# Kernel optimization log

Hardware: AMD Instinct MI355X
Metric: run time of the kernel (lower is better)

Reference implementation:

```python
import jax, jax.numpy as jnp
import numpy as np

DIN = 1024
DOUT = 1024

def setup_inputs() -> dict:
    key = jax.random.key(0)
    kx, kq, kk, kv = jax.random.split(key, 4)
    x = jax.random.normal(kx, (4, 2048, DIN), dtype=jnp.float32)
    s = 1.0 / np.sqrt(DIN)
    Wq = jax.random.uniform(kq, (DIN, DOUT), dtype=jnp.float32, minval=-s, maxval=s)
    Wk = jax.random.uniform(kk, (DIN, DOUT), dtype=jnp.float32, minval=-s, maxval=s)
    Wv = jax.random.uniform(kv, (DIN, DOUT), dtype=jnp.float32, minval=-s, maxval=s)
    return {"x": x, "Wq": Wq, "Wk": Wk, "Wv": Wv}

def reference(x, Wq, Wk, Wv):
    # q,k,v: [B, T, D]
    q = jnp.einsum('btd,de->bte', x, Wq)
    k = jnp.einsum('btd,de->bte', x, Wk)
    v = jnp.einsum('btd,de->bte', x, Wv)
    # scores: [B, T_q, T_k]; NOTE: no 1/sqrt(d) scaling in original
    scores = jnp.einsum('bqd,bkd->bqk', q, k)
    # Original applies softmax over dim=1 (the QUERY axis), faithfully kept
    weights = jax.nn.softmax(scores, axis=1)
    return jnp.einsum('bqk,bkd->bqd', weights, v)
```

## Files before the change

### kernel.cpp

```cpp
#include <hip/hip_runtime.h>

#define B_   4
#define T_   2048
#define D_   1024
#define MTOK 8192

typedef __attribute__((ext_vector_type(8))) _Float16 half8;
typedef __attribute__((ext_vector_type(4))) float    f32x4;

#define GLD(G, L) __builtin_amdgcn_global_load_lds(                       \
    (const __attribute__((address_space(1))) void*)(G),                   \
    (__attribute__((address_space(3))) void*)(L), 16, 0, 0)

#define BAR()   __builtin_amdgcn_s_barrier()
#define BARM()  asm volatile("s_barrier" ::: "memory")
#define LGKM0() do { asm volatile("s_waitcnt lgkmcnt(0)" ::: "memory");   \
                     __builtin_amdgcn_sched_barrier(0); } while (0)
#define VMW(n)  asm volatile("s_waitcnt vmcnt(" #n ")" ::: "memory")

__device__ __forceinline__ unsigned short f2h(float f) {
  return __builtin_bit_cast(unsigned short, (_Float16)f);
}
__device__ __forceinline__ float h2f(unsigned short u) {
  return (float)__builtin_bit_cast(_Float16, u);
}

__global__ __launch_bounds__(256) void tofp16_kernel(
    const float4* __restrict__ in, ushort4* __restrict__ out, int n4,
    float4* __restrict__ cs, int c4) {
  int i = blockIdx.x * 256 + threadIdx.x;
  if (i < c4) cs[i] = (float4){0.f, 0.f, 0.f, 0.f};
  if (i >= n4) return;
  float4 v = in[i];
  ushort4 h;
  h.x = f2h(v.x); h.y = f2h(v.y); h.z = f2h(v.z); h.w = f2h(v.w);
  out[i] = h;
}

__global__ __launch_bounds__(256) void wcat_t_kernel(
    const float* __restrict__ Wq, const float* __restrict__ Wk,
    const float* __restrict__ Wv, unsigned short* __restrict__ Wt) {
  __shared__ float tile[32][33];
  int z = blockIdx.z;
  const float* W = (z == 0) ? Wq : ((z == 1) ? Wk : Wv);
  int c0 = blockIdx.x * 32, r0 = blockIdx.y * 32;
  int tx = threadIdx.x & 31, ty = threadIdx.x >> 5;
  #pragma unroll
  for (int i = 0; i < 4; ++i)
    tile[ty + i * 8][tx] = W[(size_t)(r0 + ty + i * 8) * D_ + c0 + tx];
  __syncthreads();
  #pragma unroll
  for (int i = 0; i < 4; ++i) {
    float v = tile[tx][ty + i * 8];
    size_t row = (size_t)z * D_ + c0 + ty + i * 8;
    Wt[row * D_ + r0 + tx] = f2h(v);
  }
}

__global__ __launch_bounds__(256) void vtrans_kernel(
    const unsigned short* __restrict__ QKV, unsigned short* __restrict__ Vt) {
  __shared__ unsigned short tile[64][68];
  int b = blockIdx.z;
  int t0 = blockIdx.x * 64, d0 = blockIdx.y * 64;
  int l16 = threadIdx.x & 15, rr = threadIdx.x >> 4;
  const unsigned short* src =
      QKV + ((size_t)b * 2048 + t0 + rr) * 3072 + 2048 + d0 + l16 * 4;
  #pragma unroll
  for (int i = 0; i < 4; ++i) {
    ushort4 v = *(const ushort4*)(src + (size_t)i * 16 * 3072);
    *(ushort4*)&tile[rr + i * 16][l16 * 4] = v;
  }
  __syncthreads();
  unsigned short* dst = Vt + ((size_t)b * D_ + d0) * 2048 + t0;
  #pragma unroll
  for (int j = 0; j < 4; ++j) {
    int dd = rr + j * 16;
    int tt = l16 * 4;
    ushort4 v;
    v.x = tile[tt + 0][dd]; v.y = tile[tt + 1][dd];
    v.z = tile[tt + 2][dd]; v.w = tile[tt + 3][dd];
    *(ushort4*)(dst + (size_t)dd * 2048 + tt) = v;
  }
}

template <int EPI>
__global__ __launch_bounds__(512, 4) void gemm8p(
    const unsigned short* __restrict__ A, const unsigned short* __restrict__ B,
    void* __restrict__ C0, float* __restrict__ CS,
    int K, int lda, int ldb, int ldc,
    long aBatch, long bBatch, long cBatch) {
  constexpr int ABY  = 128 * 64;
  constexpr int BUFB = ABY + 16384;
  __shared__ __align__(16) char lds[2 * BUFB];

  const int z = blockIdx.z;
  A += (size_t)z * aBatch;
  B += (size_t)z * bBatch;

  const int nwg = gridDim.x * gridDim.y;
  int s = blockIdx.y * gridDim.x + blockIdx.x;
  s = (s & 7) * (nwg >> 3) + (s >> 3);
  const int bx = s % gridDim.x, by = s / gridDim.x;
  const int brow = by * 128, bcol = bx * 256;

  const int tid = threadIdx.x;
  const int wid = tid >> 6, lane = tid & 63;
  const int wr = wid >> 2, wc = wid & 3;
  const int l15 = lane & 15, g4 = lane >> 4;

  const int scol = ((lane & 3) ^ ((lane >> 3) & 3)) * 8;
  const int srow = lane >> 2;
  int aoff, adst, boffs[2], bdst[2];
  {
    int r0 = wid * 16;
    aoff = (brow + r0 + srow) * lda + scol;
    adst = r0 * 64;
    #pragma unroll
    for (int rg = 0; rg < 2; ++rg) {
      int rb = (wid >> 1) * 64 + rg * 32 + (wid & 1) * 16;
      boffs[rg] = (bcol + rb + srow) * ldb + scol;
      bdst[rg]  = ABY + rb * 64;
    }
  }

  const int rslot = (g4 ^ ((l15 >> 1) & 3)) * 16;
  int aRd[2], bRd[2];
  #pragma unroll
  for (int mh = 0; mh < 2; ++mh) {
    aRd[mh] = (wr * 64 + mh * 32 + l15) * 64 + rslot;
    bRd[mh] = ABY + (wc * 64 + mh * 32 + l15) * 64 + rslot;
  }

#define STAGE_A(bb, tt) \
    GLD(A + (size_t)(aoff + (tt) * 32), lds + (bb) * BUFB + adst)
#define STAGE_B(nh, bb, tt) \
    GLD(B + (size_t)(boffs[nh] + (tt) * 32), lds + (bb) * BUFB + bdst[nh])
#define LOAD_A(mh) do { _Pragma("unroll")                                     \
    for (int mf = 0; mf < 2; ++mf)                                            \
      ar[mf] = *(const half8*)(buf + aRd[mh] + mf * 1024); } while (0)
#define LOAD_B(dst, nh) do { _Pragma("unroll")                                \
    for (int nf = 0; nf < 2; ++nf)                                            \
      dst[nf] = *(const half8*)(buf + bRd[nh] + nf * 1024); } while (0)
#define MFMA_Q(mh, nh, br) do { _Pragma("unroll")                             \
    for (int mf = 0; mf < 2; ++mf) { _Pragma("unroll")                        \
      for (int nf = 0; nf < 2; ++nf) {                                        \
        f32x4& ac = acc[(mh) * 2 + mf][(nh) * 2 + nf];                        \
        ac = __builtin_amdgcn_mfma_f32_16x16x32_f16(ar[mf], br[nf], ac, 0, 0, 0); \
      } } } while (0)

  STAGE_A(0, 0); STAGE_B(0, 0, 0); STAGE_B(1, 0, 0);
  STAGE_A(1, 1); STAGE_B(0, 1, 1); STAGE_B(1, 1, 1);
  VMW(3);
  BAR();

  f32x4 acc[4][4] = {};
  half8 ar[2], b0r[2], b1r[2];
  const int nIter = K / 64;

  for (int it = 0; it < nIter; ++it) {
    const bool st = (it + 1 < nIter);
    #pragma unroll
    for (int h = 0; h < 2; ++h) {
      const char* buf = lds + h * BUFB;
      const int tt = 2 * it + 2 + h;
      LOAD_A(0); LOAD_B(b0r, 0);
      BAR(); LGKM0();
      __builtin_amdgcn_s_setprio(1); MFMA_Q(0, 0, b0r);
      __builtin_amdgcn_s_setprio(0); BAR();
      LOAD_B(b1r, 1);
      if (st) STAGE_B(0, h, tt);
      BAR(); LGKM0();
      __builtin_amdgcn_s_setprio(1); MFMA_Q(0, 1, b1r);
      __builtin_amdgcn_s_setprio(0); BAR();
      LOAD_A(1);
      if (st) STAGE_B(1, h, tt);
      BAR(); LGKM0();
      __builtin_amdgcn_s_setprio(1); MFMA_Q(1, 1, b1r);
      __builtin_amdgcn_s_setprio(0); BAR();
      if (st) STAGE_A(h, tt);
      BAR();
      __builtin_amdgcn_s_setprio(1); MFMA_Q(1, 0, b0r);
      __builtin_amdgcn_s_setprio(0);
      if (st) { VMW(3); } else { VMW(0); }
      BAR();
    }
  }

  if constexpr (EPI == 1) {
    unsigned short* C = (unsigned short*)C0 + (size_t)z * cBatch;
    #pragma unroll
    for (int m = 0; m < 4; ++m) {
      int rowoff = (m >> 1) * 32 + (m & 1) * 16;
      #pragma unroll
      for (int n = 0; n < 4; ++n) {
        int coloff = (n >> 1) * 32 + (n & 1) * 16;
        #pragma unroll
        for (int r = 0; r < 4; ++r) {
          int row = brow + wr * 64 + rowoff + g4 * 4 + r;
          int col = bcol + wc * 64 + coloff + l15;
          C[(size_t)row * ldc + col] = f2h(acc[m][n][r]);
        }
      }
    }
  } else {
    unsigned short* C = (unsigned short*)C0 + (size_t)z * cBatch;
    float csum[4] = {0.f, 0.f, 0.f, 0.f};
    #pragma unroll
    for (int m = 0; m < 4; ++m) {
      int rowoff = (m >> 1) * 32 + (m & 1) * 16;
      #pragma unroll
      for (int n = 0; n < 4; ++n) {
        int coloff = (n >> 1) * 32 + (n & 1) * 16;
        #pragma unroll
        for (int r = 0; r < 4; ++r) {
          int row = brow + wr * 64 + rowoff + g4 * 4 + r;
          int col = bcol + wc * 64 + coloff + l15;
          unsigned short hh = f2h(acc[m][n][r]);
          C[(size_t)row * ldc + col] = hh;
          csum[n] += __expf(h2f(hh) - 64.0f);
        }
      }
    }
    #pragma unroll
    for (int n = 0; n < 4; ++n) {
      csum[n] += __shfl_xor(csum[n], 16);
      csum[n] += __shfl_xor(csum[n], 32);
    }
    if (g4 == 0) {
      #pragma unroll
      for (int n = 0; n < 4; ++n) {
        int col = bcol + wc * 64 + (n >> 1) * 32 + (n & 1) * 16 + l15;
        unsafeAtomicAdd(CS + (size_t)z * T_ + col, csum[n]);
      }
    }
  }
#undef STAGE_A
#undef STAGE_B
#undef LOAD_A
#undef LOAD_B
#undef MFMA_Q
}

__global__ __launch_bounds__(256, 2) void gemmPV(
    const unsigned short* __restrict__ Sc, const float* __restrict__ U,
    const unsigned short* __restrict__ Bv, float* __restrict__ out) {
  constexpr int ABY  = 64 * 64;
  constexpr int BUFB = ABY + 16384;
  __shared__ __align__(16) char lds[3 * BUFB];

  const int b = blockIdx.z;
  Sc += (size_t)b * T_ * T_;
  U  += (size_t)b * T_;
  Bv += (size_t)b * D_ * T_;
  float* Co = out + (size_t)b * T_ * D_;

  const int nwg = gridDim.x * gridDim.y;
  int s = blockIdx.y * gridDim.x + blockIdx.x;
  s = (s & 7) * (nwg >> 3) + (s >> 3);
  const int bx = s % gridDim.x, by = s / gridDim.x;
  const int brow = by * 64, bcol = bx * 256;

  const int tid = threadIdx.x;
  const int wid = tid >> 6, lane = tid & 63;
  const int l15 = lane & 15, g4 = lane >> 4;

  const int arow = tid >> 2;
  const unsigned short* aSrc = Sc + (size_t)(brow + arow) * T_ + (tid & 3) * 8;
  const int awB  = arow * 64 + ((tid & 3) ^ ((tid >> 3) & 3)) * 16;
  const int ucol = (tid & 3) * 8;

  const int scol = ((lane & 3) ^ ((lane >> 3) & 3)) * 8;
  const int srow = lane >> 2;
  int boffs[4], bdst[4];
  #pragma unroll
  for (int g = 0; g < 4; ++g) {
    int rb = g * 64 + wid * 16;
    boffs[g] = (bcol + rb + srow) * T_ + scol;
    bdst[g]  = ABY + rb * 64;
  }

  const int rslot = (g4 ^ ((l15 >> 1) & 3)) * 16;
  int aRd[4], bRd[4];
  #pragma unroll
  for (int mf = 0; mf < 4; ++mf)
    aRd[mf] = (mf * 16 + l15) * 64 + rslot;
  #pragma unroll
  for (int nf = 0; nf < 4; ++nf)
    bRd[nf] = ABY + (wid * 64 + nf * 16 + l15) * 64 + rslot;

  uint4 rawA;
  float4 uva, uvb;

#define PV_BSTAGE(base, tt) do { _Pragma("unroll")                            \
    for (int g = 0; g < 4; ++g)                                               \
      GLD(Bv + (size_t)(boffs[g] + (tt) * 32), (base) + bdst[g]); } while (0)
#define PV_AISSUE(tt) do {                                                    \
    rawA = *(const uint4*)(aSrc + (size_t)(tt) * 32);                         \
    uva  = *(const float4*)(U + (tt) * 32 + ucol);                            \
    uvb  = *(const float4*)(U + (tt) * 32 + ucol + 4); } while (0)
#define PV_AWRITE(base) do {                                                  \
    const unsigned short* hp = (const unsigned short*)&rawA;                  \
    float uu[8] = {uva.x, uva.y, uva.z, uva.w, uvb.x, uvb.y, uvb.z, uvb.w};   \
    unsigned int w_[4];                                                       \
    _Pragma("unroll") for (int j = 0; j < 4; ++j) {                           \
      float w0 = __expf(h2f(hp[2 * j])     - 64.f) * uu[2 * j];               \
      float w1 = __expf(h2f(hp[2 * j + 1]) - 64.f) * uu[2 * j + 1];           \
      w_[j] = (unsigned int)f2h(w0) | ((unsigned int)f2h(w1) << 16); }        \
    *(uint4*)((base) + awB) = *(uint4*)w_; } while (0)

  char* bufA = lds;
  char* bufB = lds + BUFB;
  char* bufC = lds + 2 * BUFB;

  PV_AISSUE(0);
  PV_BSTAGE(bufA, 0);
  uint4  rawA1 = *(const uint4*)(aSrc + 32);
  float4 uva1  = *(const float4*)(U + 32 + ucol);
  float4 uvb1  = *(const float4*)(U + 32 + ucol + 4);
  PV_BSTAGE(bufB, 1);
  VMW(11);
  PV_AWRITE(bufA);
  VMW(4);
  rawA = rawA1; uva = uva1; uvb = uvb1;
  PV_AWRITE(bufB);
  asm volatile("s_waitcnt lgkmcnt(0)" ::: "memory");

  f32x4 acc[4][4] = {};
  half8 ar[4], br[4];
  const int NT = T_ / 32;

  for (int t = 0; t < NT; ++t) {
    BARM();
    const bool st = (t + 2 < NT);
    if (st) {
      PV_AISSUE(t + 2);
      PV_BSTAGE(bufC, t + 2);
    }
    #pragma unroll
    for (int mf = 0; mf < 4; ++mf)
      ar[mf] = *(const half8*)(bufA + aRd[mf]);
    #pragma unroll
    for (int nf = 0; nf < 4; ++nf)
      br[nf] = *(const half8*)(bufA + bRd[nf]);
    __builtin_amdgcn_s_setprio(1);
    #pragma unroll
    for (int mf = 0; mf < 4; ++mf)
      #pragma unroll
      for (int nf = 0; nf < 4; ++nf)
        acc[mf][nf] = __builtin_amdgcn_mfma_f32_16x16x32_f16(ar[mf], br[nf], acc[mf][nf], 0, 0, 0);
    __builtin_amdgcn_s_setprio(0);
    if (st) {
      VMW(4);
      PV_AWRITE(bufC);
      asm volatile("s_waitcnt lgkmcnt(0)" ::: "memory");
    } else if (t + 2 == NT) {
      VMW(0);
    }
    char* tmp = bufA; bufA = bufB; bufB = bufC; bufC = tmp;
  }

  #pragma unroll
  for (int mf = 0; mf < 4; ++mf)
    #pragma unroll
    for (int nf = 0; nf < 4; ++nf)
      #pragma unroll
      for (int r = 0; r < 4; ++r) {
        int row = brow + mf * 16 + g4 * 4 + r;
        int col = bcol + wid * 64 + nf * 16 + l15;
        Co[(size_t)row * D_ + col] = acc[mf][nf][r];
      }
#undef PV_BSTAGE
#undef PV_AISSUE
#undef PV_AWRITE
}

__global__ __launch_bounds__(256) void sm_stats(const float* __restrict__ cs,
                                                float* __restrict__ stats) {
  int i = blockIdx.x * 256 + threadIdx.x;
  stats[i] = 1.0f / cs[i];
}

extern "C" void kernel_launch(void* const* d_in, const int* in_sizes, int n_in,
                              void* d_out, int out_size, void* d_ws, size_t ws_size,
                              hipStream_t stream) {
  const float* x  = (const float*)d_in[0];
  const float* Wq = (const float*)d_in[1];
  const float* Wk = (const float*)d_in[2];
  const float* Wv = (const float*)d_in[3];
  float* out = (float*)d_out;

  char* ws = (char*)d_ws;
  const size_t MB = 1024ull * 1024ull;
  unsigned short* scoresh = (unsigned short*)(ws);
  unsigned short* QKVh = (unsigned short*)(ws + 32 * MB);
  unsigned short* Vt   = (unsigned short*)(ws + 80 * MB);
  unsigned short* xh   = (unsigned short*)(ws + 96 * MB);
  unsigned short* Wt   = (unsigned short*)(ws + 112 * MB);
  float* colsum = (float*)(ws + 118 * MB);
  float* stats  = (float*)(ws + 118 * MB + 64 * 1024);

  tofp16_kernel<<<MTOK * D_ / 4 / 256, 256, 0, stream>>>(
      (const float4*)x, (ushort4*)xh, MTOK * D_ / 4,
      (float4*)colsum, B_ * T_ / 4);

  wcat_t_kernel<<<dim3(32, 32, 3), 256, 0, stream>>>(Wq, Wk, Wv, Wt);

  gemm8p<1><<<dim3(3072 / 256, MTOK / 128, 1), 512, 0, stream>>>(
      xh, Wt, QKVh, nullptr, D_, D_, D_, 3072, 0, 0, 0);

  vtrans_kernel<<<dim3(T_ / 64, D_ / 64, B_), 256, 0, stream>>>(QKVh, Vt);

  gemm8p<2><<<dim3(T_ / 256, T_ / 128, B_), 512, 0, stream>>>(
      QKVh, QKVh + 1024, scoresh, colsum, D_, 3072, 3072, T_,
      (long)T_ * 3072, (long)T_ * 3072, (long)T_ * T_);

  sm_stats<<<B_ * T_ / 256, 256, 0, stream>>>(colsum, stats);

  gemmPV<<<dim3(D_ / 256, T_ / 64, B_), 256, 0, stream>>>(
      scoresh, stats, Vt, out);
}
```

Measured before the change: 198.3 us.

## Add dedicated 128x128 scores GEMM and deepen PV A-operand prefetch

Replaces the 256x128, 512-thread gemm8p instantiation for the QK^T scores with a new 256-thread 128x128-tile kernel, gemmS. It uses a three-buffer global_load_lds pipeline, targets three blocks per CU, and keeps the fused column-sum/atomic epilogue. gemmPV now prefetches the softmax-weight operand one tile further ahead into registers, using a two-tile unrolled loop with alternating register sets, so global latency is hidden behind the MFMAs. This trades more registers and a smaller tile with less reuse for better occupancy and deeper latency hiding.

```diff
diff --git a/kernel.cpp b/kernel.cpp
--- a/kernel.cpp
+++ b/kernel.cpp
@@ -186,51 +186,18 @@
     }
   }
 
-  if constexpr (EPI == 1) {
-    unsigned short* C = (unsigned short*)C0 + (size_t)z * cBatch;
-    #pragma unroll
-    for (int m = 0; m < 4; ++m) {
-      int rowoff = (m >> 1) * 32 + (m & 1) * 16;
+  unsigned short* C = (unsigned short*)C0 + (size_t)z * cBatch;
+  #pragma unroll
+  for (int m = 0; m < 4; ++m) {
+    int rowoff = (m >> 1) * 32 + (m & 1) * 16;
+    #pragma unroll
+    for (int n = 0; n < 4; ++n) {
+      int coloff = (n >> 1) * 32 + (n & 1) * 16;
       #pragma unroll
-      for (int n = 0; n < 4; ++n) {
-        int coloff = (n >> 1) * 32 + (n & 1) * 16;
-        #pragma unroll
-        for (int r = 0; r < 4; ++r) {
-          int row = brow + wr * 64 + rowoff + g4 * 4 + r;
-          int col = bcol + wc * 64 + coloff + l15;
-          C[(size_t)row * ldc + col] = f2h(acc[m][n][r]);
-        }
-      }
-    }
-  } else {
-    unsigned short* C = (unsigned short*)C0 + (size_t)z * cBatch;
-    float csum[4] = {0.f, 0.f, 0.f, 0.f};
-    #pragma unroll
-    for (int m = 0; m < 4; ++m) {
-      int rowoff = (m >> 1) * 32 + (m & 1) * 16;
-      #pragma unroll
-      for (int n = 0; n < 4; ++n) {
-        int coloff = (n >> 1) * 32 + (n & 1) * 16;
-        #pragma unroll
-        for (int r = 0; r < 4; ++r) {
-          int row = brow + wr * 64 + rowoff + g4 * 4 + r;
-          int col = bcol + wc * 64 + coloff + l15;
-          unsigned short hh = f2h(acc[m][n][r]);
-          C[(size_t)row * ldc + col] = hh;
-          csum[n] += __expf(h2f(hh) - 64.0f);
-        }
-      }
-    }
-    #pragma unroll
-    for (int n = 0; n < 4; ++n) {
-      csum[n] += __shfl_xor(csum[n], 16);
-      csum[n] += __shfl_xor(csum[n], 32);
-    }
-    if (g4 == 0) {
-      #pragma unroll
-      for (int n = 0; n < 4; ++n) {
-        int col = bcol + wc * 64 + (n >> 1) * 32 + (n & 1) * 16 + l15;
-        unsafeAtomicAdd(CS + (size_t)z * T_ + col, csum[n]);
+      for (int r = 0; r < 4; ++r) {
+        int row = brow + wr * 64 + rowoff + g4 * 4 + r;
+        int col = bcol + wc * 64 + coloff + l15;
+        C[(size_t)row * ldc + col] = f2h(acc[m][n][r]);
       }
     }
   }
@@ -239,6 +206,119 @@
 #undef LOAD_A
 #undef LOAD_B
 #undef MFMA_Q
+}
+
+__global__ __launch_bounds__(256, 3) void gemmS(
+    const unsigned short* __restrict__ A, const unsigned short* __restrict__ B,
+    unsigned short* __restrict__ C0, float* __restrict__ CS,
+    int K, int lda, int ldb, int ldc,
+    long aBatch, long bBatch, long cBatch) {
+  constexpr int ABY  = 128 * 64;
+  constexpr int BUFB = ABY + 8192;
+  __shared__ __align__(16) char lds[3 * BUFB];
+
+  const int z = blockIdx.z;
+  A += (size_t)z * aBatch;
+  B += (size_t)z * bBatch;
+
+  const int nwg = gridDim.x * gridDim.y;
+  int s = blockIdx.y * gridDim.x + blockIdx.x;
+  s = (s & 7) * (nwg >> 3) + (s >> 3);
+  const int bx = s % gridDim.x, by = s / gridDim.x;
+  const int brow = by * 128, bcol = bx * 128;
+
+  const int tid = threadIdx.x;
+  const int wid = tid >> 6, lane = tid & 63;
+  const int wr = wid >> 1, wc = wid & 1;
+  const int l15 = lane & 15, g4 = lane >> 4;
+
+  const int scol = ((lane & 3) ^ ((lane >> 3) & 3)) * 8;
+  const int srow = lane >> 2;
+  int aoffs[2], adst[2], boffs[2], bdst[2];
+  #pragma unroll
+  for (int g = 0; g < 2; ++g) {
+    int r0 = wid * 32 + g * 16;
+    aoffs[g] = (brow + r0 + srow) * lda + scol;
+    adst[g]  = r0 * 64;
+    boffs[g] = (bcol + r0 + srow) * ldb + scol;
+    bdst[g]  = ABY + r0 * 64;
+  }
+
+  const int rslot = (g4 ^ ((l15 >> 1) & 3)) * 16;
+  int aRd[4], bRd[4];
+  #pragma unroll
+  for (int mf = 0; mf < 4; ++mf)
+    aRd[mf] = (wr * 64 + mf * 16 + l15) * 64 + rslot;
+  #pragma unroll
+  for (int nf = 0; nf < 4; ++nf)
+    bRd[nf] = ABY + (wc * 64 + nf * 16 + l15) * 64 + rslot;
+
+#define S_STAGE(base, tt) do { _Pragma("unroll")                              \
+    for (int g = 0; g < 2; ++g) {                                             \
+      GLD(A + (size_t)(aoffs[g] + (tt) * 32), (base) + adst[g]);              \
+      GLD(B + (size_t)(boffs[g] + (tt) * 32), (base) + bdst[g]); } } while (0)
+
+  char* bufA = lds;
+  char* bufB = lds + BUFB;
+  char* bufC = lds + 2 * BUFB;
+
+  S_STAGE(bufA, 0);
+  S_STAGE(bufB, 1);
+  VMW(4);
+
+  f32x4 acc[4][4] = {};
+  half8 ar[4], br[4];
+  const int NT = K / 32;
+
+  for (int t = 0; t < NT; ++t) {
+    BARM();
+    const bool st = (t + 2 < NT);
+    if (st) S_STAGE(bufC, t + 2);
+    #pragma unroll
+    for (int mf = 0; mf < 4; ++mf)
+      ar[mf] = *(const half8*)(bufA + aRd[mf]);
+    #pragma unroll
+    for (int nf = 0; nf < 4; ++nf)
+      br[nf] = *(const half8*)(bufA + bRd[nf]);
+    __builtin_amdgcn_s_setprio(1);
+    #pragma unroll
+    for (int mf = 0; mf < 4; ++mf)
+      #pragma unroll
+      for (int nf = 0; nf < 4; ++nf)
+        acc[mf][nf] = __builtin_amdgcn_mfma_f32_16x16x32_f16(ar[mf], br[nf], acc[mf][nf], 0, 0, 0);
+    __builtin_amdgcn_s_setprio(0);
+    if (st)                VMW(4);
+    else if (t + 2 == NT)  VMW(0);
+    char* tmp = bufA; bufA = bufB; bufB = bufC; bufC = tmp;
+  }
+
+  unsigned short* C = C0 + (size_t)z * cBatch;
+  float csum[4] = {0.f, 0.f, 0.f, 0.f};
+  #pragma unroll
+  for (int mf = 0; mf < 4; ++mf)
+    #pragma unroll
+    for (int nf = 0; nf < 4; ++nf)
+      #pragma unroll
+      for (int r = 0; r < 4; ++r) {
+        int row = brow + wr * 64 + mf * 16 + g4 * 4 + r;
+        int col = bcol + wc * 64 + nf * 16 + l15;
+        unsigned short hh = f2h(acc[mf][nf][r]);
+        C[(size_t)row * ldc + col] = hh;
+        csum[nf] += __expf(h2f(hh) - 64.0f);
+      }
+  #pragma unroll
+  for (int nf = 0; nf < 4; ++nf) {
+    csum[nf] += __shfl_xor(csum[nf], 16);
+    csum[nf] += __shfl_xor(csum[nf], 32);
+  }
+  if (g4 == 0) {
+    #pragma unroll
+    for (int nf = 0; nf < 4; ++nf) {
+      int col = bcol + wc * 64 + nf * 16 + l15;
+      unsafeAtomicAdd(CS + (size_t)z * T_ + col, csum[nf]);
+    }
+  }
+#undef S_STAGE
 }
 
 __global__ __launch_bounds__(256, 2) void gemmPV(
@@ -288,75 +368,73 @@
   for (int nf = 0; nf < 4; ++nf)
     bRd[nf] = ABY + (wid * 64 + nf * 16 + l15) * 64 + rslot;
 
-  uint4 rawA;
-  float4 uva, uvb;
-
 #define PV_BSTAGE(base, tt) do { _Pragma("unroll")                            \
     for (int g = 0; g < 4; ++g)                                               \
       GLD(Bv + (size_t)(boffs[g] + (tt) * 32), (base) + bdst[g]); } while (0)
-#define PV_AISSUE(tt) do {                                                    \
-    rawA = *(const uint4*)(aSrc + (size_t)(tt) * 32);                         \
-    uva  = *(const float4*)(U + (tt) * 32 + ucol);                            \
-    uvb  = *(const float4*)(U + (tt) * 32 + ucol + 4); } while (0)
-#define PV_AWRITE(base) do {                                                  \
-    const unsigned short* hp = (const unsigned short*)&rawA;                  \
-    float uu[8] = {uva.x, uva.y, uva.z, uva.w, uvb.x, uvb.y, uvb.z, uvb.w};   \
+#define PV_ALOAD(rA, uA, uB, tt) do {                                         \
+    rA = *(const uint4*)(aSrc + (size_t)(tt) * 32);                           \
+    uA = *(const float4*)(U + (tt) * 32 + ucol);                              \
+    uB = *(const float4*)(U + (tt) * 32 + ucol + 4); } while (0)
+#define PV_AWRITE(base, rA, uA, uB) do {                                      \
+    const unsigned short* hp = (const unsigned short*)&rA;                    \
+    float uu[8] = {uA.x, uA.y, uA.z, uA.w, uB.x, uB.y, uB.z, uB.w};           \
     unsigned int w_[4];                                                       \
     _Pragma("unroll") for (int j = 0; j < 4; ++j) {                           \
       float w0 = __expf(h2f(hp[2 * j])     - 64.f) * uu[2 * j];               \
       float w1 = __expf(h2f(hp[2 * j + 1]) - 64.f) * uu[2 * j + 1];           \
       w_[j] = (unsigned int)f2h(w0) | ((unsigned int)f2h(w1) << 16); }        \
     *(uint4*)((base) + awB) = *(uint4*)w_; } while (0)
+#define PV_COMPUTE() do {                                                     \
+    _Pragma("unroll") for (int mf = 0; mf < 4; ++mf)                          \
+      ar[mf] = *(const half8*)(bufA + aRd[mf]);                               \
+    _Pragma("unroll") for (int nf = 0; nf < 4; ++nf)                          \
+      br[nf] = *(const half8*)(bufA + bRd[nf]);                               \
+    __builtin_amdgcn_s_setprio(1);                                            \
+    _Pragma("unroll") for (int mf = 0; mf < 4; ++mf)                          \
+      _Pragma("unroll") for (int nf = 0; nf < 4; ++nf)                        \
+        acc[mf][nf] = __builtin_amdgcn_mfma_f32_16x16x32_f16(                 \
+            ar[mf], br[nf], acc[mf][nf], 0, 0, 0);                            \
+    __builtin_amdgcn_s_setprio(0); } while (0)
+#define PV_TILE(t, rC, uCa, uCb, rN, uNa, uNb) do {                           \
+    BARM();                                                                   \
+    if ((t) + 2 < NT) PV_BSTAGE(bufC, (t) + 2);                               \
+    if ((t) + 3 < NT) PV_ALOAD(rN, uNa, uNb, (t) + 3);                        \
+    PV_COMPUTE();                                                             \
+    if ((t) + 3 < NT)      VMW(7);                                            \
+    else if ((t) + 2 < NT) VMW(4);                                            \
+    else if ((t) + 2 == NT) VMW(0);                                           \
+    if ((t) + 2 < NT) {                                                       \
+      PV_AWRITE(bufC, rC, uCa, uCb);                                          \
+      asm volatile("s_waitcnt lgkmcnt(0)" ::: "memory");                      \
+    }                                                                         \
+    { char* tmp = bufA; bufA = bufB; bufB = bufC; bufC = tmp; } } while (0)
 
   char* bufA = lds;
   char* bufB = lds + BUFB;
   char* bufC = lds + 2 * BUFB;
 
-  PV_AISSUE(0);
+  uint4 rA_E, rA_O; float4 uAa_E, uAb_E, uAa_O, uAb_O;
+
+  uint4 rA0; float4 uA0a, uA0b;
+  PV_ALOAD(rA0, uA0a, uA0b, 0);
   PV_BSTAGE(bufA, 0);
-  uint4  rawA1 = *(const uint4*)(aSrc + 32);
-  float4 uva1  = *(const float4*)(U + 32 + ucol);
-  float4 uvb1  = *(const float4*)(U + 32 + ucol + 4);
+  uint4 rA1; float4 uA1a, uA1b;
+  PV_ALOAD(rA1, uA1a, uA1b, 1);
   PV_BSTAGE(bufB, 1);
-  VMW(11);
-  PV_AWRITE(bufA);
-  VMW(4);
-  rawA = rawA1; uva = uva1; uvb = uvb1;
-  PV_AWRITE(bufB);
+  PV_ALOAD(rA_O, uAa_O, uAb_O, 2);
+  VMW(14);
+  PV_AWRITE(bufA, rA0, uA0a, uA0b);
+  VMW(7);
+  PV_AWRITE(bufB, rA1, uA1a, uA1b);
   asm volatile("s_waitcnt lgkmcnt(0)" ::: "memory");
 
   f32x4 acc[4][4] = {};
   half8 ar[4], br[4];
   const int NT = T_ / 32;
 
-  for (int t = 0; t < NT; ++t) {
-    BARM();
-    const bool st = (t + 2 < NT);
-    if (st) {
-      PV_AISSUE(t + 2);
-      PV_BSTAGE(bufC, t + 2);
-    }
-    #pragma unroll
-    for (int mf = 0; mf < 4; ++mf)
-      ar[mf] = *(const half8*)(bufA + aRd[mf]);
-    #pragma unroll
-    for (int nf = 0; nf < 4; ++nf)
-      br[nf] = *(const half8*)(bufA + bRd[nf]);
-    __builtin_amdgcn_s_setprio(1);
-    #pragma unroll
-    for (int mf = 0; mf < 4; ++mf)
-      #pragma unroll
-      for (int nf = 0; nf < 4; ++nf)
-        acc[mf][nf] = __builtin_amdgcn_mfma_f32_16x16x32_f16(ar[mf], br[nf], acc[mf][nf], 0, 0, 0);
-    __builtin_amdgcn_s_setprio(0);
-    if (st) {
-      VMW(4);
-      PV_AWRITE(bufC);
-      asm volatile("s_waitcnt lgkmcnt(0)" ::: "memory");
-    } else if (t + 2 == NT) {
-      VMW(0);
-    }
-    char* tmp = bufA; bufA = bufB; bufB = bufC; bufC = tmp;
+  for (int t = 0; t < NT; t += 2) {
+    PV_TILE(t,     rA_O, uAa_O, uAb_O, rA_E, uAa_E, uAb_E);
+    PV_TILE(t + 1, rA_E, uAa_E, uAb_E, rA_O, uAa_O, uAb_O);
   }
 
   #pragma unroll
@@ -370,8 +448,10 @@
         Co[(size_t)row * D_ + col] = acc[mf][nf][r];
       }
 #undef PV_BSTAGE
-#undef PV_AISSUE
+#undef PV_ALOAD
 #undef PV_AWRITE
+#undef PV_COMPUTE
+#undef PV_TILE
 }
 
 __global__ __launch_bounds__(256) void sm_stats(const float* __restrict__ cs,
@@ -410,7 +490,7 @@
 
   vtrans_kernel<<<dim3(T_ / 64, D_ / 64, B_), 256, 0, stream>>>(QKVh, Vt);
 
-  gemm8p<2><<<dim3(T_ / 256, T_ / 128, B_), 512, 0, stream>>>(
+  gemmS<<<dim3(T_ / 128, T_ / 128, B_), 256, 0, stream>>>(
       QKVh, QKVh + 1024, scoresh, colsum, D_, 3072, 3072, T_,
       (long)T_ * 3072, (long)T_ * 3072, (long)T_ * T_);
 
```

Measured after the change: 207.7 us. 1.05x slower.

## Transpose PV GEMM tiling so scores load straight to registers with LDS-staged output

Applied to the files above, without the earlier changes.

The PV kernel now tiles over 256 query rows by 64 output features per block. The score tiles are loaded directly into registers as the MFMA B operand, and the exp-and-scale step runs in registers, so scores are no longer staged through LDS. Only Vt is staged in LDS through a three-buffer ring, and results are transposed through LDS for coalesced float4 stores. This aims to cut LDS traffic and footprint on the larger operand and to vectorise the output writes, at the cost of uncoalesced 16-byte register loads of scores and extra barriers in the epilogue.

```diff
diff --git a/kernel.cpp b/kernel.cpp
--- a/kernel.cpp
+++ b/kernel.cpp
@@ -241,137 +241,129 @@
 #undef MFMA_Q
 }
 
-__global__ __launch_bounds__(256, 2) void gemmPV(
+__global__ __launch_bounds__(256, 2) void gemmPVt(
     const unsigned short* __restrict__ Sc, const float* __restrict__ U,
-    const unsigned short* __restrict__ Bv, float* __restrict__ out) {
-  constexpr int ABY  = 64 * 64;
-  constexpr int BUFB = ABY + 16384;
-  __shared__ __align__(16) char lds[3 * BUFB];
+    const unsigned short* __restrict__ Vt, float* __restrict__ out) {
+  constexpr int BUFB = 4096;
+  __shared__ __align__(16) char lds[34816];
 
   const int b = blockIdx.z;
   Sc += (size_t)b * T_ * T_;
   U  += (size_t)b * T_;
-  Bv += (size_t)b * D_ * T_;
+  Vt += (size_t)b * D_ * T_;
   float* Co = out + (size_t)b * T_ * D_;
 
   const int nwg = gridDim.x * gridDim.y;
   int s = blockIdx.y * gridDim.x + blockIdx.x;
   s = (s & 7) * (nwg >> 3) + (s >> 3);
   const int bx = s % gridDim.x, by = s / gridDim.x;
-  const int brow = by * 64, bcol = bx * 256;
+  const int q0 = bx * 256, d0 = by * 64;
 
   const int tid = threadIdx.x;
   const int wid = tid >> 6, lane = tid & 63;
   const int l15 = lane & 15, g4 = lane >> 4;
 
-  const int arow = tid >> 2;
-  const unsigned short* aSrc = Sc + (size_t)(brow + arow) * T_ + (tid & 3) * 8;
-  const int awB  = arow * 64 + ((tid & 3) ^ ((tid >> 3) & 3)) * 16;
-  const int ucol = (tid & 3) * 8;
-
   const int scol = ((lane & 3) ^ ((lane >> 3) & 3)) * 8;
-  const int srow = lane >> 2;
-  int boffs[4], bdst[4];
-  #pragma unroll
-  for (int g = 0; g < 4; ++g) {
-    int rb = g * 64 + wid * 16;
-    boffs[g] = (bcol + rb + srow) * T_ + scol;
-    bdst[g]  = ABY + rb * 64;
-  }
+  const int aoff = (d0 + wid * 16 + (lane >> 2)) * T_ + scol;
+  const int adst = wid * 1024;
 
   const int rslot = (g4 ^ ((l15 >> 1) & 3)) * 16;
-  int aRd[4], bRd[4];
+  int aRd[4];
   #pragma unroll
   for (int mf = 0; mf < 4; ++mf)
     aRd[mf] = (mf * 16 + l15) * 64 + rslot;
+
+  const unsigned short* bSrc[4];
   #pragma unroll
   for (int nf = 0; nf < 4; ++nf)
-    bRd[nf] = ABY + (wid * 64 + nf * 16 + l15) * 64 + rslot;
-
-  uint4 rawA;
-  float4 uva, uvb;
-
-#define PV_BSTAGE(base, tt) do { _Pragma("unroll")                            \
-    for (int g = 0; g < 4; ++g)                                               \
-      GLD(Bv + (size_t)(boffs[g] + (tt) * 32), (base) + bdst[g]); } while (0)
-#define PV_AISSUE(tt) do {                                                    \
-    rawA = *(const uint4*)(aSrc + (size_t)(tt) * 32);                         \
-    uva  = *(const float4*)(U + (tt) * 32 + ucol);                            \
-    uvb  = *(const float4*)(U + (tt) * 32 + ucol + 4); } while (0)
-#define PV_AWRITE(base) do {                                                  \
-    const unsigned short* hp = (const unsigned short*)&rawA;                  \
-    float uu[8] = {uva.x, uva.y, uva.z, uva.w, uvb.x, uvb.y, uvb.z, uvb.w};   \
-    unsigned int w_[4];                                                       \
-    _Pragma("unroll") for (int j = 0; j < 4; ++j) {                           \
-      float w0 = __expf(h2f(hp[2 * j])     - 64.f) * uu[2 * j];               \
-      float w1 = __expf(h2f(hp[2 * j + 1]) - 64.f) * uu[2 * j + 1];           \
-      w_[j] = (unsigned int)f2h(w0) | ((unsigned int)f2h(w1) << 16); }        \
-    *(uint4*)((base) + awB) = *(uint4*)w_; } while (0)
+    bSrc[nf] = Sc + (size_t)(q0 + wid * 64 + nf * 16 + l15) * T_ + g4 * 8;
+  const float* uSrc = U + g4 * 8;
+
+#define PV_CONV(bw, rW, uA, uB) do {                                          \
+    float uu[8] = {uA.x, uA.y, uA.z, uA.w, uB.x, uB.y, uB.z, uB.w};           \
+    _Pragma("unroll") for (int nf = 0; nf < 4; ++nf) {                        \
+      const unsigned short* hp = (const unsigned short*)&rW[nf];              \
+      unsigned int w_[4];                                                     \
+      _Pragma("unroll") for (int j = 0; j < 4; ++j) {                         \
+        float w0 = __expf(h2f(hp[2 * j])     - 64.f) * uu[2 * j];             \
+        float w1 = __expf(h2f(hp[2 * j + 1]) - 64.f) * uu[2 * j + 1];         \
+        w_[j] = (unsigned int)f2h(w0) | ((unsigned int)f2h(w1) << 16); }      \
+      bw[nf] = *(half8*)w_; } } while (0)
+
+#define PV_TILE(t, rWC, uaC, ubC, rWN, uaN, ubN) do {                         \
+    BARM();                                                                   \
+    if ((t) + 2 < NT)                                                         \
+      GLD(Vt + (size_t)(aoff + ((t) + 2) * 32), bufC + adst);                 \
+    if ((t) + 1 < NT) {                                                       \
+      _Pragma("unroll") for (int nf = 0; nf < 4; ++nf)                        \
+        rWN[nf] = *(const uint4*)(bSrc[nf] + ((t) + 1) * 32);                 \
+      uaN = *(const float4*)(uSrc + ((t) + 1) * 32);                          \
+      ubN = *(const float4*)(uSrc + ((t) + 1) * 32 + 4);                      \
+    }                                                                         \
+    if ((t) + 2 < NT)      VMW(7);                                            \
+    else if ((t) + 1 < NT) VMW(6);                                            \
+    else                   VMW(0);                                            \
+    half8 bw[4];                                                              \
+    PV_CONV(bw, rWC, uaC, ubC);                                               \
+    half8 ar_[4];                                                             \
+    _Pragma("unroll") for (int mf = 0; mf < 4; ++mf)                          \
+      ar_[mf] = *(const half8*)(bufA + aRd[mf]);                              \
+    LGKM0();                                                                  \
+    __builtin_amdgcn_s_setprio(1);                                            \
+    _Pragma("unroll") for (int mf = 0; mf < 4; ++mf)                          \
+      _Pragma("unroll") for (int nf = 0; nf < 4; ++nf)                        \
+        acc[mf][nf] = __builtin_amdgcn_mfma_f32_16x16x32_f16(                 \
+            ar_[mf], bw[nf], acc[mf][nf], 0, 0, 0);                           \
+    __builtin_amdgcn_s_setprio(0);                                            \
+    { char* tmp = bufA; bufA = bufB; bufB = bufC; bufC = tmp; } } while (0)
 
   char* bufA = lds;
   char* bufB = lds + BUFB;
   char* bufC = lds + 2 * BUFB;
 
-  PV_AISSUE(0);
-  PV_BSTAGE(bufA, 0);
-  uint4  rawA1 = *(const uint4*)(aSrc + 32);
-  float4 uva1  = *(const float4*)(U + 32 + ucol);
-  float4 uvb1  = *(const float4*)(U + 32 + ucol + 4);
-  PV_BSTAGE(bufB, 1);
-  VMW(11);
-  PV_AWRITE(bufA);
-  VMW(4);
-  rawA = rawA1; uva = uva1; uvb = uvb1;
-  PV_AWRITE(bufB);
-  asm volatile("s_waitcnt lgkmcnt(0)" ::: "memory");
+  uint4 rW_E[4], rW_O[4];
+  float4 uA_E, uB_E, uA_O, uB_O;
+
+  GLD(Vt + (size_t)aoff, bufA + adst);
+  GLD(Vt + (size_t)(aoff + 32), bufB + adst);
+  #pragma unroll
+  for (int nf = 0; nf < 4; ++nf) rW_E[nf] = *(const uint4*)(bSrc[nf]);
+  uA_E = *(const float4*)uSrc;
+  uB_E = *(const float4*)(uSrc + 4);
+  VMW(0);
 
   f32x4 acc[4][4] = {};
-  half8 ar[4], br[4];
   const int NT = T_ / 32;
 
-  for (int t = 0; t < NT; ++t) {
+  for (int t = 0; t < NT; t += 2) {
+    PV_TILE(t,     rW_E, uA_E, uB_E, rW_O, uA_O, uB_O);
+    PV_TILE(t + 1, rW_O, uA_O, uB_O, rW_E, uA_E, uB_E);
+  }
+
+  float* T0 = (float*)lds;
+  #pragma unroll
+  for (int h = 0; h < 2; ++h) {
     BARM();
-    const bool st = (t + 2 < NT);
-    if (st) {
-      PV_AISSUE(t + 2);
-      PV_BSTAGE(bufC, t + 2);
-    }
-    #pragma unroll
-    for (int mf = 0; mf < 4; ++mf)
-      ar[mf] = *(const half8*)(bufA + aRd[mf]);
-    #pragma unroll
-    for (int nf = 0; nf < 4; ++nf)
-      br[nf] = *(const half8*)(bufA + bRd[nf]);
-    __builtin_amdgcn_s_setprio(1);
-    #pragma unroll
-    for (int mf = 0; mf < 4; ++mf)
+    if ((wid >> 1) == h) {
+      int qloc = (wid & 1) * 64;
       #pragma unroll
-      for (int nf = 0; nf < 4; ++nf)
-        acc[mf][nf] = __builtin_amdgcn_mfma_f32_16x16x32_f16(ar[mf], br[nf], acc[mf][nf], 0, 0, 0);
-    __builtin_amdgcn_s_setprio(0);
-    if (st) {
-      VMW(4);
-      PV_AWRITE(bufC);
-      asm volatile("s_waitcnt lgkmcnt(0)" ::: "memory");
-    } else if (t + 2 == NT) {
-      VMW(0);
-    }
-    char* tmp = bufA; bufA = bufB; bufB = bufC; bufC = tmp;
-  }
-
-  #pragma unroll
-  for (int mf = 0; mf < 4; ++mf)
-    #pragma unroll
-    for (int nf = 0; nf < 4; ++nf)
-      #pragma unroll
-      for (int r = 0; r < 4; ++r) {
-        int row = brow + mf * 16 + g4 * 4 + r;
-        int col = bcol + wid * 64 + nf * 16 + l15;
-        Co[(size_t)row * D_ + col] = acc[mf][nf][r];
-      }
-#undef PV_BSTAGE
-#undef PV_AISSUE
-#undef PV_AWRITE
+      for (int mf = 0; mf < 4; ++mf)
+        #pragma unroll
+        for (int nf = 0; nf < 4; ++nf)
+          *(f32x4*)&T0[(qloc + nf * 16 + l15) * 68 + mf * 16 + g4 * 4] =
+              acc[mf][nf];
+    }
+    BARM();
+    #pragma unroll
+    for (int p = 0; p < 8; ++p) {
+      int qloc = p * 16 + (tid >> 4);
+      int dloc = (tid & 15) * 4;
+      f32x4 v = *(const f32x4*)&T0[qloc * 68 + dloc];
+      *(f32x4*)&Co[(size_t)(q0 + h * 128 + qloc) * D_ + d0 + dloc] = v;
+    }
+  }
+#undef PV_CONV
+#undef PV_TILE
 }
 
 __global__ __launch_bounds__(256) void sm_stats(const float* __restrict__ cs,
@@ -416,6 +408,6 @@
 
   sm_stats<<<B_ * T_ / 256, 256, 0, stream>>>(colsum, stats);
 
-  gemmPV<<<dim3(D_ / 256, T_ / 64, B_), 256, 0, stream>>>(
+  gemmPVt<<<dim3(T_ / 256, D_ / 64, B_), 256, 0, stream>>>(
       scoresh, stats, Vt, out);
 }
```

After: 240.2 us. +21.1%, slower.
